# Kernel optimization log

Measured on AMD Instinct MI355X. Metric: run time of the kernel, lower is better.

Reference implementation:

```python
import jax, jax.numpy as jnp
import numpy as np

N, E, G = 100000, 1600000, 256
IN_DIM, HID, H3_DIM = 21, 64, 32
NEG_SLOPE = 0.2


def _gat_layer(x, src, dst, W, a_src, a_dst, b, heads, ch):
    # PyG GATConv with add_self_loops=True, concat=True, negative_slope=0.2
    n = x.shape[0]
    h = (x @ W).reshape(n, heads, ch)                       # [N,H,C]
    a_s = jnp.einsum('nhc,hc->nh', h, a_src)                # per-node source score
    a_d = jnp.einsum('nhc,hc->nh', h, a_dst)                # per-node target score
    e = jax.nn.leaky_relu(a_s[src] + a_d[dst], NEG_SLOPE)   # [E,H]
    # segment softmax over incoming edges of each target node
    m = jax.ops.segment_max(e, dst, num_segments=n)
    m = jnp.where(jnp.isfinite(m), m, 0.0)
    m = jax.lax.stop_gradient(m)
    ex = jnp.exp(e - m[dst])
    denom = jax.ops.segment_sum(ex, dst, num_segments=n)
    alpha = ex / (denom[dst] + 1e-16)                       # [E,H]
    out = jax.ops.segment_sum(alpha[:, :, None] * h[src], dst, num_segments=n)
    return out.reshape(n, heads * ch) + b


def setup_inputs() -> dict:
    key = jax.random.key(0)
    ks = jax.random.split(key, 24)
    s = 0.1
    inp = {
        'x': jax.random.normal(ks[0], (N, IN_DIM), jnp.float32),
        'edge_index': jax.random.randint(ks[1], (2, E), 0, N, jnp.int64),
        'batch': jnp.sort(jax.random.randint(ks[2], (N,), 0, G, jnp.int64)),
        'w1': jax.random.normal(ks[3], (IN_DIM, 4 * HID), jnp.float32) * s,
        'as1': jax.random.normal(ks[4], (4, HID), jnp.float32) * s,
        'ad1': jax.random.normal(ks[5], (4, HID), jnp.float32) * s,
        'b1': jax.random.normal(ks[6], (4 * HID,), jnp.float32) * s,
        'w2': jax.random.normal(ks[7], (4 * HID, 4 * HID), jnp.float32) * s,
        'as2': jax.random.normal(ks[8], (4, HID), jnp.float32) * s,
        'ad2': jax.random.normal(ks[9], (4, HID), jnp.float32) * s,
        'b2': jax.random.normal(ks[10], (4 * HID,), jnp.float32) * s,
        'w3': jax.random.normal(ks[11], (4 * HID, H3_DIM), jnp.float32) * s,
        'as3': jax.random.normal(ks[12], (1, H3_DIM), jnp.float32) * s,
        'ad3': jax.random.normal(ks[13], (1, H3_DIM), jnp.float32) * s,
        'b3': jax.random.normal(ks[14], (H3_DIM,), jnp.float32) * s,
        # FC head 32 -> 64 -> 32 -> 1
        'fw1': jax.random.normal(ks[15], (H3_DIM, 64), jnp.float32) * s,
        'fb1': jnp.zeros((64,), jnp.float32),
        'fw2': jax.random.normal(ks[16], (64, 32), jnp.float32) * s,
        'fb2': jnp.zeros((32,), jnp.float32),
        'fw3': jax.random.normal(ks[17], (32, 1), jnp.float32) * s,
        'fb3': jnp.zeros((1,), jnp.float32),
    }
    return inp


def reference(x, edge_index, batch, w1, as1, ad1, b1, w2, as2, ad2, b2,
              w3, as3, ad3, b3, fw1, fb1, fw2, fb2, fw3, fb3):
    n = x.shape[0]
    loop = jnp.arange(n, dtype=edge_index.dtype)
    src = jnp.concatenate([edge_index[0], loop])  # add self loops (PyG default)
    dst = jnp.concatenate([edge_index[1], loop])
    h = jax.nn.elu(_gat_layer(x, src, dst, w1, as1, ad1, b1, 4, HID))
    h = jax.nn.elu(_gat_layer(h, src, dst, w2, as2, ad2, b2, 4, HID))
    h = jax.nn.elu(_gat_layer(h, src, dst, w3, as3, ad3, b3, 1, H3_DIM))
    # global mean pool over graphs
    sums = jax.ops.segment_sum(h, batch, num_segments=G)
    cnts = jax.ops.segment_sum(jnp.ones((n,), h.dtype), batch, num_segments=G)
    g = sums / jnp.maximum(cnts, 1.0)[:, None]              # [G,32]
    g = jax.nn.relu(g @ fw1 + fb1)                          # dropout is identity in eval
    g = jax.nn.relu(g @ fw2 + fb2)
    g = jax.nn.sigmoid(g @ fw3 + fb3)
    return g.squeeze(-1)
```

## Files before the change

### kernel.cpp

```cpp
#include <hip/hip_runtime.h>
#include <math.h>

typedef float f4 __attribute__((ext_vector_type(4)));
typedef float f32x4 __attribute__((ext_vector_type(4)));
typedef float f32x2 __attribute__((ext_vector_type(2)));
typedef short bf16x8 __attribute__((ext_vector_type(8)));
typedef unsigned int u32x2 __attribute__((ext_vector_type(2)));
typedef int i32x4 __attribute__((ext_vector_type(4)));
typedef unsigned short u16x4 __attribute__((ext_vector_type(4)));

__device__ __forceinline__ float lrelu(float x) { return x >= 0.f ? x : 0.2f * x; }
__device__ __forceinline__ float eluf(float x)  { return x > 0.f ? x : __expf(x) - 1.f; }

__device__ __forceinline__ float bf2f(unsigned short u) {
    union { unsigned int i; float f; } c; c.i = ((unsigned int)u) << 16; return c.f;
}
__device__ __forceinline__ unsigned short f2bf(float f) {
    union { float f; unsigned int i; } c; c.f = f;
    unsigned int r = c.i + 0x7fffu + ((c.i >> 16) & 1u);
    return (unsigned short)(r >> 16);
}
__device__ __forceinline__ unsigned char f2f8(float f) {
    return (unsigned char)(__builtin_amdgcn_cvt_pk_fp8_f32(f, f, 0u, false) & 0xffu);
}

__global__ void k_deg_pack(const int* __restrict__ edst, int* __restrict__ deg,
                           unsigned short* __restrict__ rank, int E, int DB,
                           const float* __restrict__ w2, unsigned char* __restrict__ w2p8,
                           const float* __restrict__ w3, unsigned char* __restrict__ w3p8,
                           const float* __restrict__ w1, const float* __restrict__ as1,
                           const float* __restrict__ ad1, float* __restrict__ cw) {
    int b = blockIdx.x;
    int tid = threadIdx.x;
    if (b < DB) {
        int base = (b * 256 + tid) * 4;
        if (base + 3 < E) {
            i32x4 d = *reinterpret_cast<const i32x4*>(&edst[base]);
            u16x4 r;
            r.x = (unsigned short)atomicAdd(&deg[d.x], 1);
            r.y = (unsigned short)atomicAdd(&deg[d.y], 1);
            r.z = (unsigned short)atomicAdd(&deg[d.z], 1);
            r.w = (unsigned short)atomicAdd(&deg[d.w], 1);
            *reinterpret_cast<u16x4*>(&rank[base]) = r;
        } else {
            for (int e = base; e < E; ++e)
                rank[e] = (unsigned short)atomicAdd(&deg[edst[e]], 1);
        }
    } else if (b < DB + 256) {
        int i = (b - DB) * 256 + tid;
        int k = i >> 8, c = i & 255;
        w2p8[((size_t)(k >> 3) * 256 + c) * 8 + (k & 7)] = f2f8(w2[i]);
    } else if (b < DB + 256 + 32) {
        int i = (b - DB - 256) * 256 + tid;
        int k = i >> 5, c = i & 31;
        w3p8[((size_t)(k >> 3) * 32 + c) * 8 + (k & 7)] = f2f8(w3[i]);
    } else {
        if (tid < 168) {
            int k = tid >> 3, j = tid & 7;
            int h = j >> 1;
            const float* av = (j & 1) ? ad1 : as1;
            float s = 0.f;
            for (int c = 0; c < 64; ++c)
                s = fmaf(w1[k * 256 + h * 64 + c], av[h * 64 + c], s);
            cw[k * 8 + j] = s;
        }
    }
}

__global__ __launch_bounds__(1024) void k_scan1(const int* __restrict__ deg,
                                                int* __restrict__ bsum, int N) {
    int t = threadIdx.x;
    int i = blockIdx.x * 1024 + t;
    int v = (i < N) ? deg[i] : 0;
#pragma unroll
    for (int m = 32; m; m >>= 1) v += __shfl_xor(v, m);
    __shared__ int ws[16];
    if ((t & 63) == 0) ws[t >> 6] = v;
    __syncthreads();
    if (t < 16) {
        int s = ws[t];
#pragma unroll
        for (int m = 8; m; m >>= 1) s += __shfl_xor(s, m);
        if (t == 0) bsum[blockIdx.x] = s;
    }
}

__global__ void k_scan2(int* __restrict__ bsum, int B) {
    __shared__ int sm[256];
    int t = threadIdx.x;
    int v = (t < B) ? bsum[t] : 0;
    sm[t] = v;
    __syncthreads();
    for (int d = 1; d < 256; d <<= 1) {
        int x = (t >= d) ? sm[t - d] : 0;
        __syncthreads();
        sm[t] += x;
        __syncthreads();
    }
    if (t < B) bsum[t] = sm[t] - v;
}

__global__ __launch_bounds__(1024) void k_scan3(const int* __restrict__ deg,
                                                const int* __restrict__ bsum,
                                                int* __restrict__ offs, int N) {
    __shared__ int sm[1024];
    int t = threadIdx.x;
    int i = blockIdx.x * 1024 + t;
    int v = (i < N) ? deg[i] : 0;
    sm[t] = v;
    __syncthreads();
    for (int d = 1; d < 1024; d <<= 1) {
        int x = (t >= d) ? sm[t - d] : 0;
        __syncthreads();
        sm[t] += x;
        __syncthreads();
    }
    int pref = bsum[blockIdx.x] + sm[t] - v;
    if (i < N) offs[i] = pref;
    if (i == N - 1) offs[N] = pref + v;
}

__global__ void k_scatter(const int* __restrict__ esrc, const int* __restrict__ edst,
                          const unsigned short* __restrict__ rank,
                          const int* __restrict__ offs, int* __restrict__ csr, int E) {
    int base = (blockIdx.x * 256 + threadIdx.x) * 4;
    if (base + 3 < E) {
        i32x4 s = *reinterpret_cast<const i32x4*>(&esrc[base]);
        i32x4 d = *reinterpret_cast<const i32x4*>(&edst[base]);
        u16x4 r = *reinterpret_cast<const u16x4*>(&rank[base]);
        csr[offs[d.x] + r.x] = s.x;
        csr[offs[d.y] + r.y] = s.y;
        csr[offs[d.z] + r.z] = s.z;
        csr[offs[d.w] + r.w] = s.w;
    } else {
        for (int e = base; e < E; ++e) csr[offs[edst[e]] + rank[e]] = esrc[e];
    }
}

__global__ void k_gemm1(const float* __restrict__ x, const float* __restrict__ w,
                        const float* __restrict__ cw,
                        unsigned char* __restrict__ h8, float* __restrict__ asb,
                        float* __restrict__ adb, int N) {
    int tid = threadIdx.x;
    int row0 = blockIdx.x * 8;
    __shared__ float xs[8][21];
    int nrows = min(8, N - row0);
    for (int i = tid; i < nrows * 21; i += 256) xs[i / 21][i % 21] = x[row0 * 21 + i];
    __syncthreads();
    float wreg[21];
#pragma unroll
    for (int k = 0; k < 21; ++k) wreg[k] = w[k * 256 + tid];
    for (int r = 0; r < nrows; ++r) {
        float acc = 0.f;
#pragma unroll
        for (int k = 0; k < 21; ++k) acc = fmaf(xs[r][k], wreg[k], acc);
        h8[(size_t)(row0 + r) * 256 + tid] = f2f8(acc);
    }
    if (tid < 64) {
        int r = tid >> 3, j = tid & 7;
        if (r < nrows) {
            float s = 0.f;
#pragma unroll
            for (int k = 0; k < 21; ++k) s = fmaf(xs[r][k], cw[k * 8 + j], s);
            int row = row0 + r;
            if (j & 1) adb[row * 4 + (j >> 1)] = s;
            else       asb[row * 4 + (j >> 1)] = s;
        }
    }
}

__global__ __launch_bounds__(256) void k_gemm2_mfma(
        const unsigned char* __restrict__ in8, const unsigned char* __restrict__ w2p8,
        const float* __restrict__ as2f, const float* __restrict__ ad2f,
        unsigned char* __restrict__ h8, float* __restrict__ asb,
        float* __restrict__ adb, int N) {
    int tid = threadIdx.x;
    int wave = tid >> 6, lane = tid & 63;
    int g = lane >> 4, q = lane & 15;
    int row0 = blockIdx.x * 64;

    f32x4 acc[4][4];
#pragma unroll
    for (int rg = 0; rg < 4; ++rg)
#pragma unroll
        for (int cc = 0; cc < 4; ++cc) acc[rg][cc] = (f32x4)0.f;

    const unsigned char* aptr = in8 + (size_t)(row0 + q) * 256 + g * 8;
    const unsigned char* bptr = w2p8 + (size_t)g * 2048 + q * 8 + wave * 512;

#pragma unroll
    for (int kt = 0; kt < 8; ++kt) {
        long a[4];
#pragma unroll
        for (int rg = 0; rg < 4; ++rg)
            a[rg] = *reinterpret_cast<const long*>(aptr + (size_t)rg * 16 * 256 + kt * 32);
#pragma unroll
        for (int cc = 0; cc < 4; ++cc) {
            long b = *reinterpret_cast<const long*>(bptr + (size_t)kt * 8192 + cc * 128);
#pragma unroll
            for (int rg = 0; rg < 4; ++rg)
                acc[rg][cc] = __builtin_amdgcn_mfma_f32_16x16x32_fp8_fp8(a[rg], b, acc[rg][cc], 0, 0, 0);
        }
    }

#pragma unroll
    for (int rg = 0; rg < 4; ++rg) {
#pragma unroll
        for (int cc = 0; cc < 4; ++cc) {
            int col = (wave * 4 + cc) * 16 + q;
#pragma unroll
            for (int r = 0; r < 4; ++r) {
                int row = row0 + rg * 16 + 4 * g + r;
                if (row < N) h8[(size_t)row * 256 + col] = f2f8(acc[rg][cc][r]);
            }
        }
    }

#pragma unroll
    for (int rg = 0; rg < 4; ++rg) {
        float s1[4] = {0.f, 0.f, 0.f, 0.f}, s2[4] = {0.f, 0.f, 0.f, 0.f};
#pragma unroll
        for (int cc = 0; cc < 4; ++cc) {
            int col = (wave * 4 + cc) * 16 + q;
            float ws_ = as2f[col], wd_ = ad2f[col];
#pragma unroll
            for (int r = 0; r < 4; ++r) {
                s1[r] = fmaf(acc[rg][cc][r], ws_, s1[r]);
                s2[r] = fmaf(acc[rg][cc][r], wd_, s2[r]);
            }
        }
#pragma unroll
        for (int m = 1; m < 16; m <<= 1) {
#pragma unroll
            for (int r = 0; r < 4; ++r) {
                s1[r] += __shfl_xor(s1[r], m);
                s2[r] += __shfl_xor(s2[r], m);
            }
        }
        if (q == 0) {
#pragma unroll
            for (int r = 0; r < 4; ++r) {
                int row = row0 + rg * 16 + 4 * g + r;
                if (row < N) { asb[row * 4 + wave] = s1[r]; adb[row * 4 + wave] = s2[r]; }
            }
        }
    }
}

__global__ __launch_bounds__(256) void k_gemm3_mfma(
        const unsigned char* __restrict__ in8, const unsigned char* __restrict__ w3p8,
        const float* __restrict__ as3f, const float* __restrict__ ad3f,
        unsigned short* __restrict__ h3b, float* __restrict__ asb, float* __restrict__ adb,
        int N) {
    int tid = threadIdx.x;
    int wave = tid >> 6, lane = tid & 63;
    int g = lane >> 4, q = lane & 15;
    int row0 = blockIdx.x * 64 + wave * 16;

    f32x4 acc[2];
    acc[0] = (f32x4)0.f; acc[1] = (f32x4)0.f;

    const unsigned char* aptr = in8 + (size_t)(row0 + q) * 256 + g * 8;
    const unsigned char* bptr = w3p8 + (size_t)g * 256 + q * 8;

#pragma unroll
    for (int kt = 0; kt < 8; ++kt) {
        long a = *reinterpret_cast<const long*>(aptr + kt * 32);
#pragma unroll
        for (int ct = 0; ct < 2; ++ct) {
            long b = *reinterpret_cast<const long*>(bptr + (size_t)kt * 1024 + ct * 128);
            acc[ct] = __builtin_amdgcn_mfma_f32_16x16x32_fp8_fp8(a, b, acc[ct], 0, 0, 0);
        }
    }

    float s1[4] = {0.f, 0.f, 0.f, 0.f}, s2[4] = {0.f, 0.f, 0.f, 0.f};
#pragma unroll
    for (int ct = 0; ct < 2; ++ct) {
        int col = ct * 16 + q;
        float ws_ = as3f[col], wd_ = ad3f[col];
#pragma unroll
        for (int r = 0; r < 4; ++r) {
            int row = row0 + 4 * g + r;
            if (row < N) h3b[(size_t)row * 32 + col] = f2bf(acc[ct][r]);
            s1[r] = fmaf(acc[ct][r], ws_, s1[r]);
            s2[r] = fmaf(acc[ct][r], wd_, s2[r]);
        }
    }
#pragma unroll
    for (int m = 1; m < 16; m <<= 1) {
#pragma unroll
        for (int r = 0; r < 4; ++r) {
            s1[r] += __shfl_xor(s1[r], m);
            s2[r] += __shfl_xor(s2[r], m);
        }
    }
    if (q == 0) {
#pragma unroll
        for (int r = 0; r < 4; ++r) {
            int row = row0 + 4 * g + r;
            if (row < N) { asb[row] = s1[r]; adb[row] = s2[r]; }
        }
    }
}

__global__ void k_gather256(const unsigned int* __restrict__ h8,
                            const float* __restrict__ asb, const float* __restrict__ adb,
                            const int* __restrict__ offs, const int* __restrict__ csr,
                            const float* __restrict__ bias, unsigned int* __restrict__ out8,
                            int N) {
    int tid = threadIdx.x;
    int lane = tid & 63;
    int v = blockIdx.x * 4 + (tid >> 6);
    if (v >= N) return;
    int head = lane >> 4;
    int j16 = lane & 15;
    int gbase = lane & 48;
    float ad = adb[v * 4 + head];
    float w0 = __expf(lrelu(asb[v * 4 + head] + ad));
    float den = w0;
    float a0, a1, a2, a3;
    {
        unsigned int hv = h8[(size_t)v * 64 + lane];
        f32x2 lo = __builtin_amdgcn_cvt_pk_f32_fp8(hv, false);
        f32x2 hi = __builtin_amdgcn_cvt_pk_f32_fp8(hv, true);
        a0 = w0 * lo.x; a1 = w0 * lo.y; a2 = w0 * hi.x; a3 = w0 * hi.y;
    }
    int beg = offs[v], end = offs[v + 1];
    for (int c = beg; c < end; c += 16) {
        int idx = c + j16;
        int u = 0;
        float w = 0.f;
        if (idx < end) {
            u = csr[idx];
            w = __expf(lrelu(asb[u * 4 + head] + ad));
        }
#pragma unroll
        for (int j = 0; j < 16; ++j) {
            float wj = __shfl(w, gbase | j);
            int   uj = __shfl(u, gbase | j);
            den += wj;
            unsigned int hv = h8[(size_t)uj * 64 + lane];
            f32x2 lo = __builtin_amdgcn_cvt_pk_f32_fp8(hv, false);
            f32x2 hi = __builtin_amdgcn_cvt_pk_f32_fp8(hv, true);
            a0 = fmaf(wj, lo.x, a0); a1 = fmaf(wj, lo.y, a1);
            a2 = fmaf(wj, hi.x, a2); a3 = fmaf(wj, hi.y, a3);
        }
    }
    float inv = 1.f / (den + 1e-16f);
    int f0 = 4 * lane;
    float o0 = eluf(a0 * inv + bias[f0 + 0]);
    float o1 = eluf(a1 * inv + bias[f0 + 1]);
    float o2 = eluf(a2 * inv + bias[f0 + 2]);
    float o3 = eluf(a3 * inv + bias[f0 + 3]);
    unsigned int wpk = __builtin_amdgcn_cvt_pk_fp8_f32(o0, o1, 0u, false);
    wpk = __builtin_amdgcn_cvt_pk_fp8_f32(o2, o3, wpk, true);
    __builtin_nontemporal_store(wpk, &out8[(size_t)v * 64 + lane]);
}

__global__ void k_gather32(const unsigned short* __restrict__ h, const float* __restrict__ asb,
                           const float* __restrict__ adb, const int* __restrict__ offs,
                           const int* __restrict__ csr, const float* __restrict__ bias,
                           float* __restrict__ out, int N) {
    int tid = threadIdx.x;
    int v = blockIdx.x * 8 + (tid >> 5);
    int c = tid & 31;
    int gbase = tid & 32;
    if (v >= N) return;
    float ad = adb[v];
    float w0 = __expf(lrelu(asb[v] + ad));
    float den = w0;
    float acc = w0 * bf2f(h[(size_t)v * 32 + c]);
    int beg = offs[v], end = offs[v + 1];
    for (int e0 = beg; e0 < end; e0 += 32) {
        int idx = e0 + c;
        int u = 0;
        float w = 0.f;
        if (idx < end) {
            u = csr[idx];
            w = __expf(lrelu(asb[u] + ad));
        }
#pragma unroll
        for (int j = 0; j < 32; ++j) {
            float wj = __shfl(w, gbase | j);
            int   uj = __shfl(u, gbase | j);
            den += wj;
            acc = fmaf(wj, bf2f(h[(size_t)uj * 32 + c]), acc);
        }
    }
    float o = eluf(acc / (den + 1e-16f) + bias[c]);
    __builtin_nontemporal_store(o, &out[(size_t)v * 32 + c]);
}

__global__ __launch_bounds__(256) void k_pool_head(
        const float* __restrict__ h, const int* __restrict__ batch, int N,
        const float* __restrict__ fw1, const float* __restrict__ fb1,
        const float* __restrict__ fw2, const float* __restrict__ fb2,
        const float* __restrict__ fw3, const float* __restrict__ fb3,
        float* __restrict__ out, int G) {
    int g = blockIdx.x;
    int tid = threadIdx.x;
    __shared__ int bounds[2];
    __shared__ float red[8][32];
    __shared__ float pooled[32];
    __shared__ float t1[64];
    __shared__ float t2[32];

    if (tid < 2) {
        int target = g + tid;
        int lo = 0, hi = N;
        while (lo < hi) {
            int mid = (lo + hi) >> 1;
            if (batch[mid] < target) lo = mid + 1; else hi = mid;
        }
        bounds[tid] = lo;
    }
    __syncthreads();
    int beg = bounds[0], end = bounds[1];

    int f = tid & 31, r = tid >> 5;
    float s = 0.f;
    for (int i = beg + r; i < end; i += 8) s += h[(size_t)i * 32 + f];
    red[r][f] = s;
    __syncthreads();

    if (tid < 32) {
        float t = 0.f;
#pragma unroll
        for (int k = 0; k < 8; ++k) t += red[k][tid];
        float invc = 1.f / fmaxf((float)(end - beg), 1.f);
        pooled[tid] = t * invc;
    }
    __syncthreads();

    if (tid < 64) {
        float a = fb1[tid];
#pragma unroll
        for (int k = 0; k < 32; ++k) a = fmaf(pooled[k], fw1[k * 64 + tid], a);
        t1[tid] = fmaxf(a, 0.f);
    }
    __syncthreads();
    if (tid < 32) {
        float a = fb2[tid];
#pragma unroll
        for (int k = 0; k < 64; ++k) a = fmaf(t1[k], fw2[k * 32 + tid], a);
        t2[tid] = fmaxf(a, 0.f);
    }
    __syncthreads();
    if (tid == 0) {
        float o = fb3[0];
#pragma unroll
        for (int k = 0; k < 32; ++k) o = fmaf(t2[k], fw3[k], o);
        out[g] = 1.f / (1.f + __expf(-o));
    }
}

extern "C" void kernel_launch(void* const* d_in, const int* in_sizes, int n_in,
                              void* d_out, int out_size, void* d_ws, size_t ws_size,
                              hipStream_t stream) {
    const float* x    = (const float*)d_in[0];
    const int*   ei   = (const int*)d_in[1];
    const int*   batch= (const int*)d_in[2];
    const float* w1   = (const float*)d_in[3];
    const float* as1  = (const float*)d_in[4];
    const float* ad1  = (const float*)d_in[5];
    const float* b1   = (const float*)d_in[6];
    const float* w2   = (const float*)d_in[7];
    const float* as2  = (const float*)d_in[8];
    const float* ad2  = (const float*)d_in[9];
    const float* b2   = (const float*)d_in[10];
    const float* w3   = (const float*)d_in[11];
    const float* as3  = (const float*)d_in[12];
    const float* ad3  = (const float*)d_in[13];
    const float* b3   = (const float*)d_in[14];
    const float* fw1  = (const float*)d_in[15];
    const float* fb1  = (const float*)d_in[16];
    const float* fw2  = (const float*)d_in[17];
    const float* fb2  = (const float*)d_in[18];
    const float* fw3  = (const float*)d_in[19];
    const float* fb3  = (const float*)d_in[20];
    float* outp = (float*)d_out;

    const int N = in_sizes[0] / 21;
    const int E = in_sizes[1] / 2;
    const int G = out_size;

    char* p = (char*)d_ws;
    auto alloc = [&](size_t bytes) -> void* {
        void* r = (void*)p;
        p += (bytes + 255) & ~(size_t)255;
        return r;
    };
    int*   deg  = (int*)alloc((size_t)N * 4);
    int*   offs = (int*)alloc((size_t)(N + 1) * 4);
    int*   csr  = (int*)alloc((size_t)E * 4);
    unsigned short* rank = (unsigned short*)alloc((size_t)E * 2);
    int*   bsum = (int*)alloc((size_t)256 * 4);
    unsigned char* h8  = (unsigned char*)alloc((size_t)N * 256);
    unsigned char* hb8 = (unsigned char*)alloc((size_t)N * 256);
    unsigned short* h3b = (unsigned short*)alloc((size_t)N * 32 * 2);
    float* hP   = (float*)alloc((size_t)N * 32 * 4);
    float* asb  = (float*)alloc((size_t)N * 4 * 4);
    float* adb  = (float*)alloc((size_t)N * 4 * 4);
    unsigned char* w2p8 = (unsigned char*)alloc((size_t)256 * 256);
    unsigned char* w3p8 = (unsigned char*)alloc((size_t)256 * 32);
    float* cw   = (float*)alloc((size_t)21 * 8 * 4);

    const int* esrc = ei;
    const int* edst = ei + E;

    (void)hipMemsetAsync(deg, 0, (size_t)N * 4, stream);

    const int sb = (N + 1023) / 1024;
    const int DB = (E + 1023) / 1024;
    const int SB = (E + 1023) / 1024;

    k_deg_pack<<<DB + 256 + 32 + 1, 256, 0, stream>>>(edst, deg, rank, E, DB,
                                                      w2, w2p8, w3, w3p8, w1, as1, ad1, cw);
    k_scan1<<<sb, 1024, 0, stream>>>(deg, bsum, N);
    k_scan2<<<1, 256, 0, stream>>>(bsum, sb);
    k_scan3<<<sb, 1024, 0, stream>>>(deg, bsum, offs, N);
    k_scatter<<<SB, 256, 0, stream>>>(esrc, edst, rank, offs, csr, E);

    const int gblk = (N + 63) / 64;

    k_gemm1<<<(N + 7) / 8, 256, 0, stream>>>(x, w1, cw, h8, asb, adb, N);
    k_gather256<<<(N + 3) / 4, 256, 0, stream>>>((const unsigned int*)h8, asb, adb, offs, csr, b1,
                                                 (unsigned int*)hb8, N);

    k_gemm2_mfma<<<gblk, 256, 0, stream>>>(hb8, w2p8, as2, ad2, h8, asb, adb, N);
    k_gather256<<<(N + 3) / 4, 256, 0, stream>>>((const unsigned int*)h8, asb, adb, offs, csr, b2,
                                                 (unsigned int*)hb8, N);

    k_gemm3_mfma<<<gblk, 256, 0, stream>>>(hb8, w3p8, as3, ad3, h3b, asb, adb, N);
    k_gather32<<<(N + 7) / 8, 256, 0, stream>>>(h3b, asb, adb, offs, csr, b3, hP, N);

    k_pool_head<<<G, 256, 0, stream>>>(hP, batch, N, fw1, fb1, fw2, fb2, fw3, fb3, outp, G);
}
```

Before: 421.8 us.

## Split gather256 wave into two half-waves processing alternate edges with 8-byte loads

Each 64-lane wave in the 256-feature attention gather is split into two 32-lane halves. Each half handles every other neighbor, with each lane loading 8 fp8 features (8 bytes) instead of 4. The halves' partial accumulators are merged with a cross-half shuffle, and the softmax denominator is reduced across the 16-lane edge group. This halves the serial per-edge loop length and doubles load width to raise memory-level parallelism, at the cost of extra shuffles and idle half-waves in the final write.

```diff
diff --git a/kernel.cpp b/kernel.cpp
--- a/kernel.cpp
+++ b/kernel.cpp
@@ -303,28 +303,36 @@
     }
 }
 
-__global__ void k_gather256(const unsigned int* __restrict__ h8,
+__global__ void k_gather256(const u32x2* __restrict__ h8,
                             const float* __restrict__ asb, const float* __restrict__ adb,
                             const int* __restrict__ offs, const int* __restrict__ csr,
-                            const float* __restrict__ bias, unsigned int* __restrict__ out8,
+                            const float* __restrict__ bias, u32x2* __restrict__ out8,
                             int N) {
     int tid = threadIdx.x;
     int lane = tid & 63;
     int v = blockIdx.x * 4 + (tid >> 6);
     if (v >= N) return;
-    int head = lane >> 4;
+    int hf = lane >> 5;
+    int fl = lane & 31;
+    int head = fl >> 3;
+    int gq = lane >> 4;
     int j16 = lane & 15;
-    int gbase = lane & 48;
-    float ad = adb[v * 4 + head];
-    float w0 = __expf(lrelu(asb[v * 4 + head] + ad));
-    float den = w0;
-    float a0, a1, a2, a3;
+    int sbase = head * 16 + hf;
+    float ad_w = adb[v * 4 + gq];
+    float w0 = __expf(lrelu(asb[v * 4 + head] + adb[v * 4 + head]));
+    float wself = hf ? 0.f : w0;
+    f32x2 a01, a23, a45, a67;
     {
-        unsigned int hv = h8[(size_t)v * 64 + lane];
-        f32x2 lo = __builtin_amdgcn_cvt_pk_f32_fp8(hv, false);
-        f32x2 hi = __builtin_amdgcn_cvt_pk_f32_fp8(hv, true);
-        a0 = w0 * lo.x; a1 = w0 * lo.y; a2 = w0 * hi.x; a3 = w0 * hi.y;
-    }
+        u32x2 hv = h8[(size_t)v * 32 + fl];
+        f32x2 p0 = __builtin_amdgcn_cvt_pk_f32_fp8(hv.x, false);
+        f32x2 p1 = __builtin_amdgcn_cvt_pk_f32_fp8(hv.x, true);
+        f32x2 p2 = __builtin_amdgcn_cvt_pk_f32_fp8(hv.y, false);
+        f32x2 p3 = __builtin_amdgcn_cvt_pk_f32_fp8(hv.y, true);
+        a01 = (f32x2)wself * p0; a23 = (f32x2)wself * p1;
+        a45 = (f32x2)wself * p2; a67 = (f32x2)wself * p3;
+    }
+    float denp = 0.f;
+    const u32x2* hrow = h8 + fl;
     int beg = offs[v], end = offs[v + 1];
     for (int c = beg; c < end; c += 16) {
         int idx = c + j16;
@@ -332,29 +340,47 @@
         float w = 0.f;
         if (idx < end) {
             u = csr[idx];
-            w = __expf(lrelu(asb[u * 4 + head] + ad));
-        }
-#pragma unroll
-        for (int j = 0; j < 16; ++j) {
-            float wj = __shfl(w, gbase | j);
-            int   uj = __shfl(u, gbase | j);
-            den += wj;
-            unsigned int hv = h8[(size_t)uj * 64 + lane];
-            f32x2 lo = __builtin_amdgcn_cvt_pk_f32_fp8(hv, false);
-            f32x2 hi = __builtin_amdgcn_cvt_pk_f32_fp8(hv, true);
-            a0 = fmaf(wj, lo.x, a0); a1 = fmaf(wj, lo.y, a1);
-            a2 = fmaf(wj, hi.x, a2); a3 = fmaf(wj, hi.y, a3);
-        }
-    }
-    float inv = 1.f / (den + 1e-16f);
-    int f0 = 4 * lane;
-    float o0 = eluf(a0 * inv + bias[f0 + 0]);
-    float o1 = eluf(a1 * inv + bias[f0 + 1]);
-    float o2 = eluf(a2 * inv + bias[f0 + 2]);
-    float o3 = eluf(a3 * inv + bias[f0 + 3]);
-    unsigned int wpk = __builtin_amdgcn_cvt_pk_fp8_f32(o0, o1, 0u, false);
-    wpk = __builtin_amdgcn_cvt_pk_fp8_f32(o2, o3, wpk, true);
-    __builtin_nontemporal_store(wpk, &out8[(size_t)v * 64 + lane]);
+            w = __expf(lrelu(asb[u * 4 + gq] + ad_w));
+        }
+        denp += w;
+#pragma unroll
+        for (int j = 0; j < 8; ++j) {
+            float wj = __shfl(w, sbase + 2 * j);
+            int   uj = __shfl(u, sbase + 2 * j);
+            u32x2 hv = hrow[(size_t)uj * 32];
+            f32x2 p0 = __builtin_amdgcn_cvt_pk_f32_fp8(hv.x, false);
+            f32x2 p1 = __builtin_amdgcn_cvt_pk_f32_fp8(hv.x, true);
+            f32x2 p2 = __builtin_amdgcn_cvt_pk_f32_fp8(hv.y, false);
+            f32x2 p3 = __builtin_amdgcn_cvt_pk_f32_fp8(hv.y, true);
+            a01 += (f32x2)wj * p0; a23 += (f32x2)wj * p1;
+            a45 += (f32x2)wj * p2; a67 += (f32x2)wj * p3;
+        }
+    }
+#pragma unroll
+    for (int m = 1; m < 16; m <<= 1) denp += __shfl_xor(denp, m);
+    float den = __shfl(denp, head * 16);
+    a01.x += __shfl_xor(a01.x, 32); a01.y += __shfl_xor(a01.y, 32);
+    a23.x += __shfl_xor(a23.x, 32); a23.y += __shfl_xor(a23.y, 32);
+    a45.x += __shfl_xor(a45.x, 32); a45.y += __shfl_xor(a45.y, 32);
+    a67.x += __shfl_xor(a67.x, 32); a67.y += __shfl_xor(a67.y, 32);
+    if (hf == 0) {
+        float inv = 1.f / (den + w0 + 1e-16f);
+        int f0 = 8 * fl;
+        float o0 = eluf(a01.x * inv + bias[f0 + 0]);
+        float o1 = eluf(a01.y * inv + bias[f0 + 1]);
+        float o2 = eluf(a23.x * inv + bias[f0 + 2]);
+        float o3 = eluf(a23.y * inv + bias[f0 + 3]);
+        float o4 = eluf(a45.x * inv + bias[f0 + 4]);
+        float o5 = eluf(a45.y * inv + bias[f0 + 5]);
+        float o6 = eluf(a67.x * inv + bias[f0 + 6]);
+        float o7 = eluf(a67.y * inv + bias[f0 + 7]);
+        unsigned int lo = __builtin_amdgcn_cvt_pk_fp8_f32(o0, o1, 0u, false);
+        lo = __builtin_amdgcn_cvt_pk_fp8_f32(o2, o3, lo, true);
+        unsigned int hi = __builtin_amdgcn_cvt_pk_fp8_f32(o4, o5, 0u, false);
+        hi = __builtin_amdgcn_cvt_pk_fp8_f32(o6, o7, hi, true);
+        u32x2 o; o.x = lo; o.y = hi;
+        __builtin_nontemporal_store(o, &out8[(size_t)v * 32 + fl]);
+    }
 }
 
 __global__ void k_gather32(const unsigned short* __restrict__ h, const float* __restrict__ asb,
@@ -524,12 +550,12 @@
     const int gblk = (N + 63) / 64;
 
     k_gemm1<<<(N + 7) / 8, 256, 0, stream>>>(x, w1, cw, h8, asb, adb, N);
-    k_gather256<<<(N + 3) / 4, 256, 0, stream>>>((const unsigned int*)h8, asb, adb, offs, csr, b1,
-                                                 (unsigned int*)hb8, N);
+    k_gather256<<<(N + 3) / 4, 256, 0, stream>>>((const u32x2*)h8, asb, adb, offs, csr, b1,
+                                                 (u32x2*)hb8, N);
 
     k_gemm2_mfma<<<gblk, 256, 0, stream>>>(hb8, w2p8, as2, ad2, h8, asb, adb, N);
-    k_gather256<<<(N + 3) / 4, 256, 0, stream>>>((const unsigned int*)h8, asb, adb, offs, csr, b2,
-                                                 (unsigned int*)hb8, N);
+    k_gather256<<<(N + 3) / 4, 256, 0, stream>>>((const u32x2*)h8, asb, adb, offs, csr, b2,
+                                                 (u32x2*)hb8, N);
 
     k_gemm3_mfma<<<gblk, 256, 0, stream>>>(hb8, w3p8, as3, ad3, h3b, asb, adb, N);
     k_gather32<<<(N + 7) / 8, 256, 0, stream>>>(h3b, asb, adb, offs, csr, b3, hP, N);
```

Result: no change. 422.8 us (+0.2%).
